# Kernel optimization log

Hardware: AMD Instinct MI355X
Metric: run time of the kernel (lower is better)

Reference implementation:

```python
import jax, jax.numpy as jnp
import numpy as np

D_BINS = 59          # cfg.cam_d
BEV_H, BEV_W = 128, 128


def setup_inputs() -> dict:
    key = jax.random.key(0)
    k = jax.random.split(key, 7)
    B, N, Cin, H, W = 4, 6, 256, 16, 44
    C = 80  # cfg.cam_bev_c
    img_feats = jax.random.normal(k[0], (B, N, Cin, H, W), dtype=jnp.float32)
    rots = jax.random.normal(k[1], (B, N, 3, 3), dtype=jnp.float32)
    trans = jax.random.normal(k[2], (B, N, 3), dtype=jnp.float32)
    intrins = jax.random.normal(k[3], (B, N, 3, 3), dtype=jnp.float32)
    # 1x1 conv == per-pixel linear layer: weight (D+C, Cin), bias (D+C,)
    w_depth = jax.random.normal(k[4], (D_BINS + C, Cin), dtype=jnp.float32) / np.sqrt(Cin)
    b_depth = jnp.zeros((D_BINS + C,), dtype=jnp.float32)
    # projected BEV grid indices (what get_geometry produces via randint)
    geom = jax.random.randint(k[5], (B, N, D_BINS, H, W, 2), 0, BEV_H, dtype=jnp.int32)
    return {"img_feats": img_feats, "rots": rots, "trans": trans,
            "intrins": intrins, "w_depth": w_depth, "b_depth": b_depth,
            "geom": geom}


def reference(img_feats, rots, trans, intrins, w_depth, b_depth, geom):
    B, N, Cin, H, W = img_feats.shape
    C = w_depth.shape[0] - D_BINS
    # depth_net: 1x1 conv -> (B, N, D+C, H, W)
    x = jnp.einsum('bnchw,oc->bnohw', img_feats, w_depth) + b_depth[None, None, :, None, None]
    depth = jax.nn.softmax(x[:, :, :D_BINS], axis=2)          # (B,N,D,H,W)
    context = x[:, :, D_BINS:]                                 # (B,N,C,H,W)
    # outer product: (B,N,D,C,H,W) -> (B,N,D,H,W,C)
    frustum = depth[:, :, :, None] * context[:, :, None]
    frustum = jnp.transpose(frustum, (0, 1, 2, 4, 5, 3))
    # voxel pooling: scatter-add frustum points into BEV grid by geom indices
    cell = geom[..., 0] * BEV_W + geom[..., 1]                 # (B,N,D,H,W)
    flat_idx = (jnp.arange(B, dtype=jnp.int32)[:, None] * (BEV_H * BEV_W)
                + cell.reshape(B, -1)).reshape(-1)
    bev = jax.ops.segment_sum(frustum.reshape(-1, C), flat_idx,
                              num_segments=B * BEV_H * BEV_W)
    return bev.reshape(B, BEV_H, BEV_W, C).transpose(0, 3, 1, 2)  # (B,C,bev_h,bev_w)
```

## Files before the change

kernel.cpp:

```cpp
#include <hip/hip_runtime.h>
#include <hip/hip_bf16.h>
#include <math.h>

#define D_BINS 59
#define CTX    80
#define O_TOT  139
#define K_CIN  256
#define PIXELS 704
#define BNPAIR 24
#define BEVHW  16384
#define NBATCH 4
#define NPOINT (BNPAIR * D_BINS * PIXELS)
#define NPIX   (BNPAIR * PIXELS)

#define NTILE   128
#define NBUCKET (NBATCH * NTILE)
#define TCELLS  128

#define PIXB    128
#define NBLK    (NPIX / PIXB)
#define EPB     (PIXB * D_BINS)

#define CAP     2816
#define CAPP    (CAP + TCELLS * 7)

#define XDEPTH_OFF 0
#define CTX_OFF    (XDEPTH_OFF + NPOINT)
#define CNTMAT_OFF (CTX_OFF + BNPAIR * PIXELS * CTX)
#define OFSMAT_OFF (CNTMAT_OFF + NBLK * NBUCKET)
#define PLIST_OFF  (OFSMAT_OFF + NBLK * NBUCKET)

__global__ __launch_bounds__(256) void gemm_kernel(
    const float* __restrict__ img,
    const float* __restrict__ w,
    const float* __restrict__ bias,
    float* __restrict__ xdepth,
    __hip_bfloat16* __restrict__ ctx)
{
    __shared__ float As[16][64];
    __shared__ float Bs[16][64];

    const int tid = threadIdx.x;
    const int tx  = tid & 15;
    const int ty  = tid >> 4;
    const int bn  = blockIdx.z;
    const int o0  = blockIdx.y * 64;
    const int p0  = blockIdx.x * 64;

    const float* imgbn = img + (size_t)bn * K_CIN * PIXELS;

    float acc[4][4];
#pragma unroll
    for (int i = 0; i < 4; ++i)
#pragma unroll
        for (int j = 0; j < 4; ++j) acc[i][j] = 0.f;

    const int a_ol = tid >> 2;
    const int a_kc = (tid & 3) * 4;
    const int b_kl = tid >> 4;
    const int b_p4 = (tid & 15) * 4;

    for (int kt = 0; kt < K_CIN; kt += 16) {
        {
            const int o = o0 + a_ol;
            float4 v = make_float4(0.f, 0.f, 0.f, 0.f);
            if (o < O_TOT) v = *(const float4*)&w[(size_t)o * K_CIN + kt + a_kc];
            As[a_kc + 0][a_ol] = v.x;
            As[a_kc + 1][a_ol] = v.y;
            As[a_kc + 2][a_ol] = v.z;
            As[a_kc + 3][a_ol] = v.w;
        }
        *(float4*)&Bs[b_kl][b_p4] =
            *(const float4*)&imgbn[(size_t)(kt + b_kl) * PIXELS + p0 + b_p4];
        __syncthreads();

#pragma unroll
        for (int kk = 0; kk < 16; ++kk) {
            const float4 a = *(const float4*)&As[kk][ty * 4];
            const float4 b = *(const float4*)&Bs[kk][tx * 4];
            const float av[4] = {a.x, a.y, a.z, a.w};
            const float bv[4] = {b.x, b.y, b.z, b.w};
#pragma unroll
            for (int i = 0; i < 4; ++i)
#pragma unroll
                for (int j = 0; j < 4; ++j)
                    acc[i][j] += av[i] * bv[j];
        }
        __syncthreads();
    }

#pragma unroll
    for (int i = 0; i < 4; ++i) {
        const int o = o0 + ty * 4 + i;
        if (o >= O_TOT) continue;
        const float bv = bias[o];
        if (o < D_BINS) {
            float4 r = make_float4(acc[i][0] + bv, acc[i][1] + bv,
                                   acc[i][2] + bv, acc[i][3] + bv);
            *(float4*)&xdepth[((size_t)bn * D_BINS + o) * PIXELS + p0 + tx * 4] = r;
        } else {
            const int c = o - D_BINS;
            __hip_bfloat16* dst = ctx + ((size_t)bn * PIXELS + p0 + tx * 4) * CTX + c;
#pragma unroll
            for (int j = 0; j < 4; ++j)
                dst[(size_t)j * CTX] = __float2bfloat16(acc[i][j] + bv);
        }
    }
}

__global__ __launch_bounds__(256) void fill_kernel(
    const float* __restrict__ xdepth,
    const int*   __restrict__ geom,
    uint2*       __restrict__ plist,
    int*         __restrict__ cntmat,
    int*         __restrict__ ofsmat)
{
    __shared__ unsigned short cache[D_BINS][PIXB];
    __shared__ float red[2][PIXB];
    __shared__ int lh[NBUCKET];
    __shared__ int lofs[NBUCKET];
    __shared__ int lcur[NBUCKET];
    __shared__ int s[256];

    const int tid = threadIdx.x;
    const int px  = tid & (PIXB - 1);
    const int h   = tid >> 7;
    const int pix = blockIdx.x * PIXB + px;
    const int bn  = pix / PIXELS;
    const int pp  = pix - bn * PIXELS;
    const int b   = bn / 6;
    const int d0  = h * 30;

    if (tid < NBUCKET) { lh[tid] = 0; lh[tid + 256] = 0; }
    __syncthreads();

    const float* base = xdepth + (size_t)bn * D_BINS * PIXELS + pp;
    float v[30];
    float lm = -INFINITY;
#pragma unroll
    for (int i = 0; i < 30; ++i) {
        const int d = d0 + i;
        v[i] = (d < D_BINS) ? base[(size_t)d * PIXELS] : -INFINITY;
        lm = fmaxf(lm, v[i]);
    }
    red[h][px] = lm;
    __syncthreads();
    const float gm = fmaxf(red[0][px], red[1][px]);
    __syncthreads();
    float ls = 0.f;
#pragma unroll
    for (int i = 0; i < 30; ++i) {
        v[i] = __expf(v[i] - gm);
        ls += v[i];
    }
    red[h][px] = ls;
    __syncthreads();
    const float inv = 1.f / (red[0][px] + red[1][px]);
#pragma unroll
    for (int i = 0; i < 30; ++i) v[i] *= inv;

    const int2* g2 = (const int2*)geom;
#pragma unroll
    for (int i = 0; i < 30; ++i) {
        const int d = d0 + i;
        if (d < D_BINS) {
            const int2 g = g2[((size_t)(bn * D_BINS + d)) * PIXELS + pp];
            const int bucket = b * NTILE + (g.x >> 3) * 8 + (g.y >> 4);
            const int cell   = (g.x & 7) * 16 + (g.y & 15);
            cache[d][px] = (unsigned short)((bucket << 7) | cell);
            atomicAdd(&lh[bucket], 1);
        }
    }
    __syncthreads();

    const int v0 = lh[2 * tid];
    const int v1 = lh[2 * tid + 1];
    const int p  = v0 + v1;
    s[tid] = p;
    __syncthreads();
#pragma unroll
    for (int off = 1; off < 256; off <<= 1) {
        int t = (tid >= off) ? s[tid - off] : 0;
        __syncthreads();
        s[tid] += t;
        __syncthreads();
    }
    const int excl = s[tid] - p;
    lofs[2 * tid]     = excl;
    lofs[2 * tid + 1] = excl + v0;
    lcur[2 * tid]     = 0;
    lcur[2 * tid + 1] = 0;
    cntmat[(size_t)blockIdx.x * NBUCKET + 2 * tid]     = v0;
    cntmat[(size_t)blockIdx.x * NBUCKET + 2 * tid + 1] = v1;
    ofsmat[(size_t)blockIdx.x * NBUCKET + 2 * tid]     = excl;
    ofsmat[(size_t)blockIdx.x * NBUCKET + 2 * tid + 1] = excl + v0;
    __syncthreads();

    uint2* dst = plist + (size_t)blockIdx.x * EPB;
    const unsigned ctxoff = (unsigned)((bn * PIXELS + pp) * CTX);
#pragma unroll
    for (int i = 0; i < 30; ++i) {
        const int d = d0 + i;
        if (d < D_BINS) {
            const unsigned u = cache[d][px];
            const int bucket = (int)(u >> 7);
            const int pos = lofs[bucket] + atomicAdd(&lcur[bucket], 1);
            dst[pos] = make_uint2(__float_as_uint(v[i]), (ctxoff << 7) | (u & 127u));
        }
    }
}

__global__ __launch_bounds__(1024) void gather_kernel(
    const uint2* __restrict__ plist,
    const int*   __restrict__ cntmat,
    const int*   __restrict__ ofsmat,
    const unsigned short* __restrict__ ctx,
    float*       __restrict__ out)
{
    __shared__ float sacc[CTX][TCELLS + 1];
    __shared__ uint2 bufB[CAPP];
    __shared__ int sg[256];
    __shared__ int segcnt[NBLK], segofs[NBLK];
    __shared__ int cellcnt[TCELLS], celloff[TCELLS], cellcur[TCELLS], sc[TCELLS];
    uint2* bufA = (uint2*)sacc;

    const int tid    = threadIdx.x;
    const int wv     = tid >> 6;
    const int lane   = tid & 63;
    const int bucket = blockIdx.x;

    if (tid < 256) {
        const int c = (tid < NBLK) ? cntmat[(size_t)tid * NBUCKET + bucket] : 0;
        sg[tid] = c;
        if (tid < NBLK) segcnt[tid] = c;
    }
    __syncthreads();
#pragma unroll
    for (int off = 1; off < 256; off <<= 1) {
        int t = (tid < 256 && tid >= off) ? sg[tid - off] : 0;
        __syncthreads();
        if (tid < 256) sg[tid] += t;
        __syncthreads();
    }
    if (tid < NBLK) segofs[tid] = sg[tid] - segcnt[tid];
    __syncthreads();
    const int total = sg[255];

    for (int blk = wv; blk < NBLK; blk += 16) {
        const int n = segcnt[blk];
        if (!n) continue;
        const int dstb = segofs[blk];
        const uint2* sp = plist + (size_t)blk * EPB + ofsmat[(size_t)blk * NBUCKET + bucket];
        for (int i = lane; i < n; i += 64) {
            const int d = dstb + i;
            if (d < CAP) bufA[d] = sp[i];
        }
    }
    const int ncap = (total < CAP) ? total : CAP;
    __syncthreads();

    if (tid < TCELLS) cellcnt[tid] = 0;
    __syncthreads();
    for (int i = tid; i < ncap; i += 1024)
        atomicAdd(&cellcnt[bufA[i].y & 127u], 1);
    __syncthreads();
    if (tid < TCELLS) sc[tid] = (cellcnt[tid] + 7) & ~7;
    __syncthreads();
#pragma unroll
    for (int off = 1; off < TCELLS; off <<= 1) {
        int t = (tid < TCELLS && tid >= off) ? sc[tid - off] : 0;
        __syncthreads();
        if (tid < TCELLS) sc[tid] += t;
        __syncthreads();
    }
    if (tid < TCELLS) {
        celloff[tid] = sc[tid] - ((cellcnt[tid] + 7) & ~7);
        cellcur[tid] = 0;
    }
    __syncthreads();
    const int padtotal = sc[TCELLS - 1];
    for (int i = tid; i < padtotal; i += 1024) bufB[i] = make_uint2(0u, 0u);
    __syncthreads();
    for (int i = tid; i < ncap; i += 1024) {
        const uint2 e = bufA[i];
        const int c = (int)(e.y & 127u);
        bufB[celloff[c] + atomicAdd(&cellcur[c], 1)] = e;
    }
    __syncthreads();

    for (int c = wv; c < TCELLS; c += 16) {
        const int s0 = celloff[c];
        const int pc = (cellcnt[c] + 7) & ~7;
        float a0 = 0.f, a1 = 0.f;
        for (int i = 0; i < pc; i += 8) {
            uint2 e[8];
#pragma unroll
            for (int r = 0; r < 8; ++r) e[r] = bufB[s0 + i + r];
            if (lane < 40) {
                unsigned u[8];
#pragma unroll
                for (int r = 0; r < 8; ++r)
                    u[r] = *(const unsigned*)(ctx + (e[r].y >> 7) + 2 * lane);
#pragma unroll
                for (int r = 0; r < 8; ++r) {
                    const float d  = __uint_as_float(e[r].x);
                    const float f0 = __uint_as_float(u[r] << 16);
                    const float f1 = __uint_as_float(u[r] & 0xffff0000u);
                    a0 += d * f0;
                    a1 += d * f1;
                }
            }
        }
        if (lane < 40) {
            sacc[2 * lane][c]     = a0;
            sacc[2 * lane + 1][c] = a1;
        }
    }

    if (total > CAP) {
        for (int blk = 0; blk < NBLK; ++blk) {
            const int dstb = segofs[blk];
            const int n    = segcnt[blk];
            if (dstb + n <= CAP) continue;
            const uint2* sp = plist + (size_t)blk * EPB + ofsmat[(size_t)blk * NBUCKET + bucket];
            const int i0 = (CAP > dstb) ? (CAP - dstb) : 0;
            for (int i = i0; i < n; ++i) {
                const uint2 e = sp[i];
                const int c = (int)(e.y & 127u);
                if ((c & 15) == wv && lane < 40) {
                    const unsigned u = *(const unsigned*)(ctx + (e.y >> 7) + 2 * lane);
                    const float dep = __uint_as_float(e.x);
                    sacc[2 * lane][c]     += dep * __uint_as_float(u << 16);
                    sacc[2 * lane + 1][c] += dep * __uint_as_float(u & 0xffff0000u);
                }
            }
        }
    }
    __syncthreads();

    const int b  = bucket >> 7;
    const int tl = bucket & 127;
    const int tr = tl >> 3;
    const int tc = tl & 7;
    const int c0  = tid >> 4;
    const int col = tid & 15;
#pragma unroll
    for (int cc = c0; cc < CTX; cc += 64) {
#pragma unroll
        for (int r = 0; r < 8; ++r) {
            out[((size_t)(b * CTX + cc)) * BEVHW + (tr * 8 + r) * 128 + tc * 16 + col]
                = sacc[cc][r * 16 + col];
        }
    }
}

extern "C" void kernel_launch(void* const* d_in, const int* in_sizes, int n_in,
                              void* d_out, int out_size, void* d_ws, size_t ws_size,
                              hipStream_t stream)
{
    const float* img  = (const float*)d_in[0];
    const float* w    = (const float*)d_in[4];
    const float* bias = (const float*)d_in[5];
    const int*   geom = (const int*)d_in[6];
    float*       out  = (float*)d_out;

    float* ws     = (float*)d_ws;
    float* xdepth = ws + XDEPTH_OFF;
    __hip_bfloat16* ctx = (__hip_bfloat16*)(ws + CTX_OFF);
    int*   cntmat = (int*)(ws + CNTMAT_OFF);
    int*   ofsmat = (int*)(ws + OFSMAT_OFF);
    uint2* plist  = (uint2*)(ws + PLIST_OFF);

    {
        dim3 grid(11, 3, BNPAIR);
        gemm_kernel<<<grid, 256, 0, stream>>>(img, w, bias, xdepth, ctx);
    }
    fill_kernel<<<NBLK, 256, 0, stream>>>(xdepth, geom, plist, cntmat, ofsmat);

    gather_kernel<<<NBUCKET, 1024, 0, stream>>>(plist, cntmat, ofsmat,
                                                (const unsigned short*)ctx, out);
}
```

Measured before the change: 157.8 us.

## Fuse depth softmax and bucket fill into GEMM epilogue, drop fill kernel

The GEMM blocks that compute depth-bin rows (blockIdx.y==0, rows 0-63, which covers all 59 depth bins) now do the softmax, read geom, build per-block tile histograms and write the sorted point list straight from registers. This removes the xdepth round trip and the separate fill kernel launch. Buckets are now per-batch tiles (128 instead of 512), and the gather kernel scans 66 segments per batch instead of 264. In exchange, only one third of the GEMM blocks carry the heavier epilogue, which adds load imbalance and extra syncs inside the GEMM.

```diff
diff --git a/kernel.cpp b/kernel.cpp
--- a/kernel.cpp
+++ b/kernel.cpp
@@ -10,41 +10,45 @@
 #define BNPAIR 24
 #define BEVHW  16384
 #define NBATCH 4
-#define NPOINT (BNPAIR * D_BINS * PIXELS)
-#define NPIX   (BNPAIR * PIXELS)
 
 #define NTILE   128
 #define NBUCKET (NBATCH * NTILE)
 #define TCELLS  128
 
-#define PIXB    128
-#define NBLK    (NPIX / PIXB)
-#define EPB     (PIXB * D_BINS)
+#define NBLK    264
+#define SEGS    66
+#define EPB     (64 * D_BINS)
 
 #define CAP     2816
 #define CAPP    (CAP + TCELLS * 7)
 
-#define XDEPTH_OFF 0
-#define CTX_OFF    (XDEPTH_OFF + NPOINT)
-#define CNTMAT_OFF (CTX_OFF + BNPAIR * PIXELS * CTX)
-#define OFSMAT_OFF (CNTMAT_OFF + NBLK * NBUCKET)
-#define PLIST_OFF  (OFSMAT_OFF + NBLK * NBUCKET)
-
-__global__ __launch_bounds__(256) void gemm_kernel(
+#define CTX_OFF    0
+#define CTX_F      (BNPAIR * PIXELS * CTX / 2)
+#define CNTMAT_OFF (CTX_OFF + CTX_F)
+#define OFSMAT_OFF (CNTMAT_OFF + NBLK * NTILE)
+#define PLIST_OFF  (OFSMAT_OFF + NBLK * NTILE)
+
+__global__ __launch_bounds__(256) void gemm_fused(
     const float* __restrict__ img,
     const float* __restrict__ w,
     const float* __restrict__ bias,
-    float* __restrict__ xdepth,
-    __hip_bfloat16* __restrict__ ctx)
+    const int*   __restrict__ geom,
+    __hip_bfloat16* __restrict__ ctx,
+    uint2*       __restrict__ plist,
+    int*         __restrict__ cntmat,
+    int*         __restrict__ ofsmat)
 {
     __shared__ float As[16][64];
     __shared__ float Bs[16][64];
+    __shared__ float red[16][64];
+    __shared__ int lh[NTILE], lofs[NTILE], lcur[NTILE], sscan[NTILE];
 
     const int tid = threadIdx.x;
     const int tx  = tid & 15;
     const int ty  = tid >> 4;
     const int bn  = blockIdx.z;
-    const int o0  = blockIdx.y * 64;
+    const int by  = blockIdx.y;
+    const int o0  = by * 64;
     const int p0  = blockIdx.x * 64;
 
     const float* imgbn = img + (size_t)bn * K_CIN * PIXELS;
@@ -89,123 +93,138 @@
         __syncthreads();
     }
 
-#pragma unroll
-    for (int i = 0; i < 4; ++i) {
-        const int o = o0 + ty * 4 + i;
-        if (o >= O_TOT) continue;
-        const float bv = bias[o];
-        if (o < D_BINS) {
-            float4 r = make_float4(acc[i][0] + bv, acc[i][1] + bv,
-                                   acc[i][2] + bv, acc[i][3] + bv);
-            *(float4*)&xdepth[((size_t)bn * D_BINS + o) * PIXELS + p0 + tx * 4] = r;
-        } else {
+    if (by == 0) {
+        float bvv[4];
+#pragma unroll
+        for (int i = 0; i < 4; ++i) bvv[i] = bias[ty * 4 + i];
+#pragma unroll
+        for (int i = 0; i < 4; ++i)
+#pragma unroll
+            for (int j = 0; j < 4; ++j) acc[i][j] += bvv[i];
+
+        float pm[4] = {-INFINITY, -INFINITY, -INFINITY, -INFINITY};
+#pragma unroll
+        for (int i = 0; i < 4; ++i) {
+            if (ty * 4 + i < D_BINS) {
+#pragma unroll
+                for (int j = 0; j < 4; ++j) pm[j] = fmaxf(pm[j], acc[i][j]);
+            }
+        }
+#pragma unroll
+        for (int j = 0; j < 4; ++j) red[ty][tx * 4 + j] = pm[j];
+        __syncthreads();
+        float gm[4] = {-INFINITY, -INFINITY, -INFINITY, -INFINITY};
+        for (int t = 0; t < 15; ++t) {
+            const float4 r = *(const float4*)&red[t][tx * 4];
+            gm[0] = fmaxf(gm[0], r.x); gm[1] = fmaxf(gm[1], r.y);
+            gm[2] = fmaxf(gm[2], r.z); gm[3] = fmaxf(gm[3], r.w);
+        }
+        __syncthreads();
+        float ps[4] = {0.f, 0.f, 0.f, 0.f};
+#pragma unroll
+        for (int i = 0; i < 4; ++i) {
+            if (ty * 4 + i < D_BINS) {
+#pragma unroll
+                for (int j = 0; j < 4; ++j) {
+                    const float e = __expf(acc[i][j] - gm[j]);
+                    acc[i][j] = e;
+                    ps[j] += e;
+                }
+            }
+        }
+#pragma unroll
+        for (int j = 0; j < 4; ++j) red[ty][tx * 4 + j] = (ty < 15) ? ps[j] : 0.f;
+        if (tid < NTILE) lh[tid] = 0;
+        __syncthreads();
+        float gs[4] = {0.f, 0.f, 0.f, 0.f};
+        for (int t = 0; t < 15; ++t) {
+            const float4 r = *(const float4*)&red[t][tx * 4];
+            gs[0] += r.x; gs[1] += r.y; gs[2] += r.z; gs[3] += r.w;
+        }
+        float inv[4];
+#pragma unroll
+        for (int j = 0; j < 4; ++j) inv[j] = 1.f / gs[j];
+
+        const int2* g2 = (const int2*)geom;
+        unsigned bc[4][4];
+#pragma unroll
+        for (int i = 0; i < 4; ++i) {
+            const int o = ty * 4 + i;
+            if (o < D_BINS) {
+                const size_t gidx = ((size_t)(bn * D_BINS + o)) * PIXELS + p0 + tx * 4;
+                const int4 ga = *(const int4*)&g2[gidx];
+                const int4 gb = *(const int4*)&g2[gidx + 2];
+                const int gx[4] = {ga.x, ga.z, gb.x, gb.z};
+                const int gy[4] = {ga.y, ga.w, gb.y, gb.w};
+#pragma unroll
+                for (int j = 0; j < 4; ++j) {
+                    const int tile = (gx[j] >> 3) * 8 + (gy[j] >> 4);
+                    const int cell = (gx[j] & 7) * 16 + (gy[j] & 15);
+                    bc[i][j] = (unsigned)((tile << 7) | cell);
+                    atomicAdd(&lh[tile], 1);
+                }
+            }
+        }
+        __syncthreads();
+
+        if (tid < NTILE) sscan[tid] = lh[tid];
+        __syncthreads();
+#pragma unroll
+        for (int off = 1; off < NTILE; off <<= 1) {
+            const int t = (tid < NTILE && tid >= off) ? sscan[tid - off] : 0;
+            __syncthreads();
+            if (tid < NTILE) sscan[tid] += t;
+            __syncthreads();
+        }
+        const int blk = bn * 11 + blockIdx.x;
+        if (tid < NTILE) {
+            const int excl = sscan[tid] - lh[tid];
+            lofs[tid] = excl;
+            lcur[tid] = 0;
+            cntmat[(size_t)blk * NTILE + tid] = lh[tid];
+            ofsmat[(size_t)blk * NTILE + tid] = excl;
+        }
+        __syncthreads();
+
+        uint2* dst = plist + (size_t)blk * EPB;
+#pragma unroll
+        for (int j = 0; j < 4; ++j) {
+            const unsigned ctxoff = (unsigned)((bn * PIXELS + p0 + tx * 4 + j) * CTX);
+#pragma unroll
+            for (int i = 0; i < 4; ++i) {
+                const int o = ty * 4 + i;
+                if (o < D_BINS) {
+                    const unsigned u = bc[i][j];
+                    const int t = (int)(u >> 7);
+                    const int pos = lofs[t] + atomicAdd(&lcur[t], 1);
+                    dst[pos] = make_uint2(__float_as_uint(acc[i][j] * inv[j]),
+                                          (ctxoff << 7) | (u & 127u));
+                }
+            }
+        }
+
+#pragma unroll
+        for (int i = 0; i < 4; ++i) {
+            const int o = ty * 4 + i;
+            if (o >= D_BINS) {
+                const int c = o - D_BINS;
+                __hip_bfloat16* cdst = ctx + ((size_t)bn * PIXELS + p0 + tx * 4) * CTX + c;
+#pragma unroll
+                for (int j = 0; j < 4; ++j)
+                    cdst[(size_t)j * CTX] = __float2bfloat16(acc[i][j]);
+            }
+        }
+    } else {
+#pragma unroll
+        for (int i = 0; i < 4; ++i) {
+            const int o = o0 + ty * 4 + i;
+            if (o >= O_TOT) continue;
+            const float bvv = bias[o];
             const int c = o - D_BINS;
-            __hip_bfloat16* dst = ctx + ((size_t)bn * PIXELS + p0 + tx * 4) * CTX + c;
+            __hip_bfloat16* cdst = ctx + ((size_t)bn * PIXELS + p0 + tx * 4) * CTX + c;
 #pragma unroll
             for (int j = 0; j < 4; ++j)
-                dst[(size_t)j * CTX] = __float2bfloat16(acc[i][j] + bv);
-        }
-    }
-}
-
-__global__ __launch_bounds__(256) void fill_kernel(
-    const float* __restrict__ xdepth,
-    const int*   __restrict__ geom,
-    uint2*       __restrict__ plist,
-    int*         __restrict__ cntmat,
-    int*         __restrict__ ofsmat)
-{
-    __shared__ unsigned short cache[D_BINS][PIXB];
-    __shared__ float red[2][PIXB];
-    __shared__ int lh[NBUCKET];
-    __shared__ int lofs[NBUCKET];
-    __shared__ int lcur[NBUCKET];
-    __shared__ int s[256];
-
-    const int tid = threadIdx.x;
-    const int px  = tid & (PIXB - 1);
-    const int h   = tid >> 7;
-    const int pix = blockIdx.x * PIXB + px;
-    const int bn  = pix / PIXELS;
-    const int pp  = pix - bn * PIXELS;
-    const int b   = bn / 6;
-    const int d0  = h * 30;
-
-    if (tid < NBUCKET) { lh[tid] = 0; lh[tid + 256] = 0; }
-    __syncthreads();
-
-    const float* base = xdepth + (size_t)bn * D_BINS * PIXELS + pp;
-    float v[30];
-    float lm = -INFINITY;
-#pragma unroll
-    for (int i = 0; i < 30; ++i) {
-        const int d = d0 + i;
-        v[i] = (d < D_BINS) ? base[(size_t)d * PIXELS] : -INFINITY;
-        lm = fmaxf(lm, v[i]);
-    }
-    red[h][px] = lm;
-    __syncthreads();
-    const float gm = fmaxf(red[0][px], red[1][px]);
-    __syncthreads();
-    float ls = 0.f;
-#pragma unroll
-    for (int i = 0; i < 30; ++i) {
-        v[i] = __expf(v[i] - gm);
-        ls += v[i];
-    }
-    red[h][px] = ls;
-    __syncthreads();
-    const float inv = 1.f / (red[0][px] + red[1][px]);
-#pragma unroll
-    for (int i = 0; i < 30; ++i) v[i] *= inv;
-
-    const int2* g2 = (const int2*)geom;
-#pragma unroll
-    for (int i = 0; i < 30; ++i) {
-        const int d = d0 + i;
-        if (d < D_BINS) {
-            const int2 g = g2[((size_t)(bn * D_BINS + d)) * PIXELS + pp];
-            const int bucket = b * NTILE + (g.x >> 3) * 8 + (g.y >> 4);
-            const int cell   = (g.x & 7) * 16 + (g.y & 15);
-            cache[d][px] = (unsigned short)((bucket << 7) | cell);
-            atomicAdd(&lh[bucket], 1);
-        }
-    }
-    __syncthreads();
-
-    const int v0 = lh[2 * tid];
-    const int v1 = lh[2 * tid + 1];
-    const int p  = v0 + v1;
-    s[tid] = p;
-    __syncthreads();
-#pragma unroll
-    for (int off = 1; off < 256; off <<= 1) {
-        int t = (tid >= off) ? s[tid - off] : 0;
-        __syncthreads();
-        s[tid] += t;
-        __syncthreads();
-    }
-    const int excl = s[tid] - p;
-    lofs[2 * tid]     = excl;
-    lofs[2 * tid + 1] = excl + v0;
-    lcur[2 * tid]     = 0;
-    lcur[2 * tid + 1] = 0;
-    cntmat[(size_t)blockIdx.x * NBUCKET + 2 * tid]     = v0;
-    cntmat[(size_t)blockIdx.x * NBUCKET + 2 * tid + 1] = v1;
-    ofsmat[(size_t)blockIdx.x * NBUCKET + 2 * tid]     = excl;
-    ofsmat[(size_t)blockIdx.x * NBUCKET + 2 * tid + 1] = excl + v0;
-    __syncthreads();
-
-    uint2* dst = plist + (size_t)blockIdx.x * EPB;
-    const unsigned ctxoff = (unsigned)((bn * PIXELS + pp) * CTX);
-#pragma unroll
-    for (int i = 0; i < 30; ++i) {
-        const int d = d0 + i;
-        if (d < D_BINS) {
-            const unsigned u = cache[d][px];
-            const int bucket = (int)(u >> 7);
-            const int pos = lofs[bucket] + atomicAdd(&lcur[bucket], 1);
-            dst[pos] = make_uint2(__float_as_uint(v[i]), (ctxoff << 7) | (u & 127u));
+                cdst[(size_t)j * CTX] = __float2bfloat16(acc[i][j] + bvv);
         }
     }
 }
@@ -219,8 +238,8 @@
 {
     __shared__ float sacc[CTX][TCELLS + 1];
     __shared__ uint2 bufB[CAPP];
-    __shared__ int sg[256];
-    __shared__ int segcnt[NBLK], segofs[NBLK];
+    __shared__ int sg[128];
+    __shared__ int segcnt[SEGS], segofs[SEGS];
     __shared__ int cellcnt[TCELLS], celloff[TCELLS], cellcur[TCELLS], sc[TCELLS];
     uint2* bufA = (uint2*)sacc;
 
@@ -228,29 +247,33 @@
     const int wv     = tid >> 6;
     const int lane   = tid & 63;
     const int bucket = blockIdx.x;
-
-    if (tid < 256) {
-        const int c = (tid < NBLK) ? cntmat[(size_t)tid * NBUCKET + bucket] : 0;
+    const int b      = bucket >> 7;
+    const int tile   = bucket & 127;
+    const int blk0   = b * SEGS;
+
+    if (tid < 128) {
+        const int c = (tid < SEGS) ? cntmat[(size_t)(blk0 + tid) * NTILE + tile] : 0;
         sg[tid] = c;
-        if (tid < NBLK) segcnt[tid] = c;
-    }
-    __syncthreads();
-#pragma unroll
-    for (int off = 1; off < 256; off <<= 1) {
-        int t = (tid < 256 && tid >= off) ? sg[tid - off] : 0;
-        __syncthreads();
-        if (tid < 256) sg[tid] += t;
-        __syncthreads();
-    }
-    if (tid < NBLK) segofs[tid] = sg[tid] - segcnt[tid];
-    __syncthreads();
-    const int total = sg[255];
-
-    for (int blk = wv; blk < NBLK; blk += 16) {
-        const int n = segcnt[blk];
+        if (tid < SEGS) segcnt[tid] = c;
+    }
+    __syncthreads();
+#pragma unroll
+    for (int off = 1; off < 128; off <<= 1) {
+        const int t = (tid < 128 && tid >= off) ? sg[tid - off] : 0;
+        __syncthreads();
+        if (tid < 128) sg[tid] += t;
+        __syncthreads();
+    }
+    if (tid < SEGS) segofs[tid] = sg[tid] - segcnt[tid];
+    __syncthreads();
+    const int total = sg[127];
+
+    for (int sgi = wv; sgi < SEGS; sgi += 16) {
+        const int n = segcnt[sgi];
         if (!n) continue;
-        const int dstb = segofs[blk];
-        const uint2* sp = plist + (size_t)blk * EPB + ofsmat[(size_t)blk * NBUCKET + bucket];
+        const int dstb = segofs[sgi];
+        const uint2* sp = plist + (size_t)(blk0 + sgi) * EPB
+                          + ofsmat[(size_t)(blk0 + sgi) * NTILE + tile];
         for (int i = lane; i < n; i += 64) {
             const int d = dstb + i;
             if (d < CAP) bufA[d] = sp[i];
@@ -268,7 +291,7 @@
     __syncthreads();
 #pragma unroll
     for (int off = 1; off < TCELLS; off <<= 1) {
-        int t = (tid < TCELLS && tid >= off) ? sc[tid - off] : 0;
+        const int t = (tid < TCELLS && tid >= off) ? sc[tid - off] : 0;
         __syncthreads();
         if (tid < TCELLS) sc[tid] += t;
         __syncthreads();
@@ -318,11 +341,12 @@
     }
 
     if (total > CAP) {
-        for (int blk = 0; blk < NBLK; ++blk) {
-            const int dstb = segofs[blk];
-            const int n    = segcnt[blk];
+        for (int sgi = 0; sgi < SEGS; ++sgi) {
+            const int dstb = segofs[sgi];
+            const int n    = segcnt[sgi];
             if (dstb + n <= CAP) continue;
-            const uint2* sp = plist + (size_t)blk * EPB + ofsmat[(size_t)blk * NBUCKET + bucket];
+            const uint2* sp = plist + (size_t)(blk0 + sgi) * EPB
+                              + ofsmat[(size_t)(blk0 + sgi) * NTILE + tile];
             const int i0 = (CAP > dstb) ? (CAP - dstb) : 0;
             for (int i = i0; i < n; ++i) {
                 const uint2 e = sp[i];
@@ -338,7 +362,6 @@
     }
     __syncthreads();
 
-    const int b  = bucket >> 7;
     const int tl = bucket & 127;
     const int tr = tl >> 3;
     const int tc = tl & 7;
@@ -365,7 +388,6 @@
     float*       out  = (float*)d_out;
 
     float* ws     = (float*)d_ws;
-    float* xdepth = ws + XDEPTH_OFF;
     __hip_bfloat16* ctx = (__hip_bfloat16*)(ws + CTX_OFF);
     int*   cntmat = (int*)(ws + CNTMAT_OFF);
     int*   ofsmat = (int*)(ws + OFSMAT_OFF);
@@ -373,10 +395,9 @@
 
     {
         dim3 grid(11, 3, BNPAIR);
-        gemm_kernel<<<grid, 256, 0, stream>>>(img, w, bias, xdepth, ctx);
-    }
-    fill_kernel<<<NBLK, 256, 0, stream>>>(xdepth, geom, plist, cntmat, ofsmat);
-
+        gemm_fused<<<grid, 256, 0, stream>>>(img, w, bias, geom, ctx,
+                                             plist, cntmat, ofsmat);
+    }
     gather_kernel<<<NBUCKET, 1024, 0, stream>>>(plist, cntmat, ofsmat,
                                                 (const unsigned short*)ctx, out);
 }
```

Result: faster. 146.2 us (-7.3%).
